# Kernel tuning notes

Measured on AMD Instinct MI355X. Metric: run time of the kernel, lower is better.

Reference implementation:

```python
import jax, jax.numpy as jnp
import numpy as np

B, N, D, DV, FS, SE, TPH = 4096, 50, 128, 8, 4, 20, 64
NEG = -1e9
C_CLIP = 10.0  # pointer Attention use_tanh with C=10


def setup_inputs():
    key = jax.random.key(0)
    ks = jax.random.split(key, 24)
    r = lambda i, shape, s=1.0: jax.random.normal(ks[i], shape, jnp.float32) * s
    return dict(
        decoder_input=r(0, (B, D)),
        h0=r(1, (B, D)),
        c0=r(2, (B, D)),
        V_reach_mask=jnp.zeros((B, N), bool),
        start_idx=jax.random.randint(ks[3], (B,), 0, N),
        V=r(4, (B, N, DV)),
        b_E=r(5, (B, N, N)),
        b_E_abs=r(6, (B, N, N)),
        context_update=r(7, (N, B, D)),
        H_update=r(8, (B, N, D - 2)),
        start_fea=r(9, (B, FS)),
        # LSTMCell params (torch gate order i,f,g,o)
        W_ih=r(10, (4 * D, D), 0.05), W_hh=r(11, (4 * D, D), 0.05),
        b_ih=jnp.zeros(4 * D), b_hh=jnp.zeros(4 * D),
        # glimpse Attention
        gWq=r(12, (D, D), 0.05), gbq=jnp.zeros(D),
        gWr=r(13, (D, D), 0.05), gbr=jnp.zeros(D), gv=r(14, (D,), 0.05),
        # pointer Attention
        pWq=r(15, (D, D), 0.05), pbq=jnp.zeros(D),
        pWr=r(16, (D, D), 0.05), pbr=jnp.zeros(D), pv=r(17, (D,), 0.05),
        # step embedding table [max_task_num+1, 20]
        step_table=r(18, (N + 1, SE), 0.05),
        # net_TP MLP: Linear(40,64)+ReLU+Linear(64,1)
        tp_W1=r(19, (2 * DV + FS + SE, TPH), 0.05), tp_b1=jnp.zeros(TPH),
        tp_W2=r(20, (TPH, 1), 0.05), tp_b2=jnp.zeros(1),
    )


def _mask_modify(m):
    # if a row is all True, un-mask the last column
    return m.at[:, -1].set(jnp.where(m.all(axis=1), False, m[:, -1]))


def _decode(decoder_input, h0, c0, V, context_update, start_fea,
            W_ih, W_hh, b_ih, b_hh,
            gWq, gbq, gWr, gbr, gv, pWq, pbq, pWr, pbr, pv,
            step_table, tp_W1, tp_b1, tp_W2, tp_b2,
            V_reach_mask, start_idx):
    ar_b = jnp.arange(B)
    # project_ref (1x1 conv) on the fixed context: precompute once
    e_g = jnp.einsum('de,nbe->bnd', gWr, context_update) + gbr  # [B,N,D]
    e_p = jnp.einsum('de,nbe->bnd', pWr, context_update) + pbr  # [B,N,D]

    def step(carry, t):
        h, c, mask, prev, last, x = carry
        scat = mask.at[ar_b, prev].set(True)
        m = jnp.where(t == 0, _mask_modify(mask), _mask_modify(scat))
        # LSTMCell
        gates = x @ W_ih.T + b_ih + h @ W_hh.T + b_hh
        i_, f_, g_, o_ = jnp.split(gates, 4, axis=-1)
        c2 = jax.nn.sigmoid(f_) * c + jax.nn.sigmoid(i_) * jnp.tanh(g_)
        h2 = jax.nn.sigmoid(o_) * jnp.tanh(c2)
        # glimpse (n_glimpses=1, masked)
        qg = h2 @ gWq.T + gbq
        ug = jnp.einsum('d,bnd->bn', gv, jnp.tanh(qg[:, None, :] + e_g))
        ug = jnp.where(m, NEG, ug)
        gl = jnp.einsum('bnd,bn->bd', e_g, jax.nn.softmax(ug, axis=1))
        # pointer (tanh-clipped, masked)
        qp = gl @ pWq.T + pbq
        up = jnp.einsum('d,bnd->bn', pv, jnp.tanh(qp[:, None, :] + e_p))
        logits = jnp.where(m, NEG, C_CLIP * jnp.tanh(up))
        log_p = jax.nn.log_softmax(logits, axis=1)
        idxs = jnp.argmax(log_p, axis=1)
        # time-prediction features + MLP
        se = jnp.broadcast_to(step_table[t], (B, SE))
        tp_in = jnp.concatenate([V[ar_b, last], V[ar_b, idxs], start_fea, se], axis=1)
        pred = jax.nn.relu(tp_in @ tp_W1 + tp_b1) @ tp_W2 + tp_b2  # [B,1]
        # rp_update_features: next decoder input gathered from fixed context
        x2 = context_update[idxs, ar_b]
        return (h2, c2, m, idxs, idxs, x2), (log_p, idxs, pred[:, 0])

    init = (h0, c0, V_reach_mask, jnp.zeros(B, jnp.int32),
            start_idx.astype(jnp.int32), decoder_input)
    _, (lp, sel, pt) = jax.lax.scan(step, init, jnp.arange(N))
    return jnp.transpose(lp, (1, 0, 2)), sel.T, pt.T  # [B,T,N],[B,T],[B,T]


def reference(decoder_input, h0, c0, V_reach_mask, start_idx, V, b_E, b_E_abs,
              context_update, H_update, start_fea,
              W_ih, W_hh, b_ih, b_hh,
              gWq, gbq, gWr, gbr, gv, pWq, pbq, pWr, pbr, pv,
              step_table, tp_W1, tp_b1, tp_W2, tp_b2):
    log_probs, selections, pred_t = _decode(
        decoder_input, h0, c0, V, context_update, start_fea,
        W_ih, W_hh, b_ih, b_hh,
        gWq, gbq, gWr, gbr, gv, pWq, pbq, pWr, pbr, pv,
        step_table, tp_W1, tp_b1, tp_W2, tp_b2,
        V_reach_mask, start_idx)
    # (output_prob, selections, time_duration_pred, pred_eta)
    return log_probs, selections, pred_t, pred_t[..., None]
```

## Files before the change

### kernel.cpp

```cpp
#include <hip/hip_runtime.h>
#include <math.h>

#define B_   4096
#define N_   50
#define D_   128
#define DV_  8
#define FS_  4
#define SE_  20
#define TPH_ 64
#define NEGV (-1e9f)
#define G_   16
#define NBLK (B_ / G_)

__device__ __forceinline__ float frcp_(float x) { return __builtin_amdgcn_rcpf(x); }
__device__ __forceinline__ float ftanh_(float x) {
    float e = __expf(2.f * x);
    return 1.f - 2.f * frcp_(e + 1.f);
}
__device__ __forceinline__ float fsig_(float x) {
    return frcp_(1.f + __expf(-x));
}
__device__ __forceinline__ float wsum_(float v) {
#pragma unroll
    for (int m = 1; m < 64; m <<= 1) v += __shfl_xor(v, m);
    return v;
}

__global__ __launch_bounds__(256) void proj_kernel(
    const float* __restrict__ W,
    const float* __restrict__ bias,
    const float* __restrict__ cu,
    float* __restrict__ outp)
{
    __shared__ __align__(16) float scu[20][128];
    __shared__ float sb[128];
    const int tid = threadIdx.x;
    if (tid < 128) sb[tid] = bias[tid];
    const int d  = tid & 127;
    const int rq = tid >> 7;
    const float* wrow = W + d * 128;
    const int r0 = blockIdx.x * 200;
    for (int it = 0; it < 10; ++it) {
        const int rbase = r0 + it * 20;
        __syncthreads();
        for (int i = tid; i < 20 * 128; i += 256) {
            int rr = i >> 7, e = i & 127;
            int r = rbase + rr;
            int b = r / 50, n = r - b * 50;
            scu[rr][e] = cu[((size_t)n * B_ + b) * D_ + e];
        }
        __syncthreads();
        float acc[10];
#pragma unroll
        for (int k = 0; k < 10; ++k) acc[k] = 0.f;
        const int rr0 = rq * 10;
        for (int e = 0; e < 128; e += 4) {
            float4 w4 = *(const float4*)&wrow[e];
#pragma unroll
            for (int k = 0; k < 10; ++k) {
                float4 c4 = *(const float4*)&scu[rr0 + k][e];
                acc[k] += w4.x * c4.x + w4.y * c4.y + w4.z * c4.z + w4.w * c4.w;
            }
        }
        float bv = sb[d];
#pragma unroll
        for (int k = 0; k < 10; ++k)
            outp[(size_t)(rbase + rr0 + k) * D_ + d] = acc[k] + bv;
    }
}

__global__ __launch_bounds__(256) void transpose_kernel(
    const float* __restrict__ in, float* __restrict__ out, int R, int C)
{
    int idx = blockIdx.x * 256 + threadIdx.x;
    if (idx < R * C) {
        int r = idx / C, c = idx - r * C;
        out[c * R + r] = in[idx];
    }
}

#define PF_ 10

__global__ __launch_bounds__(1024, 4) void decode_kernel(
    const float* __restrict__ dec_in,
    const float* __restrict__ h0,
    const float* __restrict__ c0,
    const unsigned char* __restrict__ vmask,
    const int* __restrict__ start_idx,
    const float* __restrict__ V,
    const float* __restrict__ cu,
    const float* __restrict__ start_fea,
    const float* __restrict__ W_ih,
    const float* __restrict__ W_hh,
    const float* __restrict__ b_ih, const float* __restrict__ b_hh,
    const float* __restrict__ gWq, const float* __restrict__ gbq,
    const float* __restrict__ gv,
    const float* __restrict__ pWq, const float* __restrict__ pbq,
    const float* __restrict__ pv,
    const float* __restrict__ step_table,
    const float* __restrict__ tpW1, const float* __restrict__ tpb1,
    const float* __restrict__ tpW2, const float* __restrict__ tpb2,
    const float* __restrict__ e_g, const float* __restrict__ e_p,
    const float* __restrict__ wtI,
    const float* __restrict__ wtH,
    const float* __restrict__ gqT,
    const float* __restrict__ pqT,
    const int use_t,
    float* __restrict__ outp)
{
    __shared__ __align__(16) float sH[G_][D_];
    __shared__ __align__(16) float sC[G_][D_];
    __shared__ __align__(16) float sX[G_][D_];
    __shared__ __align__(16) float sU[G_ * 512];
    __shared__ __align__(16) float sP2[G_ * 512];
    __shared__ float sBias[512];
    __shared__ __align__(16) float sGbq[128];
    __shared__ __align__(16) float sPbq[128];
    __shared__ __align__(16) float sGv[128];
    __shared__ __align__(16) float sPv[128];
    __shared__ float sSF[G_][FS_];
    __shared__ unsigned long long sMaskC[G_];
    __shared__ int sPrev[G_], sLast[G_];

    const int tid = threadIdx.x;
    const int b0  = blockIdx.x * G_;

    for (int i = tid; i < G_ * D_; i += 1024) {
        int g = i >> 7, d = i & 127;
        size_t src = (size_t)(b0 + g) * D_ + d;
        sH[g][d] = h0[src];
        sC[g][d] = c0[src];
        sX[g][d] = dec_in[src];
    }
    if (tid < 512)       sBias[tid]      = b_ih[tid] + b_hh[tid];
    else if (tid < 640)  sGbq[tid - 512] = gbq[tid - 512];
    else if (tid < 768)  sPbq[tid - 640] = pbq[tid - 640];
    else if (tid < 896)  sGv[tid - 768]  = gv[tid - 768];
    else                 sPv[tid - 896]  = pv[tid - 896];
    if (tid < G_ * FS_) {
        int g = tid >> 2, k = tid & 3;
        sSF[g][k] = start_fea[(size_t)(b0 + g) * FS_ + k];
    }
    if (tid < G_) {
        unsigned long long mk = 0ull;
        const unsigned char* mrow = vmask + (size_t)(b0 + tid) * N_;
        for (int n = 0; n < N_; ++n)
            if (mrow[n]) mk |= (1ull << n);
        sMaskC[tid] = mk;
        sPrev[tid]  = 0;
        sLast[tid]  = start_idx[b0 + tid];
    }
    __syncthreads();

    const unsigned long long FULL = (1ull << N_) - 1ull;

    for (int t = 0; t < N_; ++t) {
        if (tid < G_) {
            unsigned long long mk = sMaskC[tid];
            if (t > 0) mk |= (1ull << sPrev[tid]);
            if ((mk & FULL) == FULL) mk &= ~(1ull << (N_ - 1));
            sMaskC[tid] = mk;
        }
        if (use_t) {
            const int j  = tid & 511;
            const int eh = tid >> 9;
            const int ebase = eh * 64;
            const float* wI = wtI + j;
            const float* wH = wtH + j;
            float acc[16];
#pragma unroll
            for (int g = 0; g < 16; ++g) acc[g] = 0.f;
#pragma unroll 2
            for (int ec = 0; ec < 64; ec += 4) {
                const int e = ebase + ec;
                float wi0 = wI[(size_t)(e + 0) * 512], wi1 = wI[(size_t)(e + 1) * 512];
                float wi2 = wI[(size_t)(e + 2) * 512], wi3 = wI[(size_t)(e + 3) * 512];
                float wh0 = wH[(size_t)(e + 0) * 512], wh1 = wH[(size_t)(e + 1) * 512];
                float wh2 = wH[(size_t)(e + 2) * 512], wh3 = wH[(size_t)(e + 3) * 512];
#pragma unroll
                for (int g = 0; g < 16; ++g) {
                    float4 x4 = *(const float4*)&sX[g][e];
                    float4 h4 = *(const float4*)&sH[g][e];
                    acc[g] += wi0 * x4.x + wi1 * x4.y + wi2 * x4.z + wi3 * x4.w
                            + wh0 * h4.x + wh1 * h4.y + wh2 * h4.z + wh3 * h4.w;
                }
            }
            if (eh == 0) {
                float bb = sBias[j];
#pragma unroll
                for (int g = 0; g < 16; ++g) sU[g * 512 + j] = acc[g] + bb;
            } else {
#pragma unroll
                for (int g = 0; g < 16; ++g) sP2[g * 512 + j] = acc[g];
            }
        } else {
            const int j  = tid & 511;
            const int gh = tid >> 9;
            const int gbase = gh * 8;
            const float* wih = W_ih + (size_t)j * 128;
            const float* whh = W_hh + (size_t)j * 128;
            float acc[8];
#pragma unroll
            for (int g = 0; g < 8; ++g) acc[g] = 0.f;
            for (int e = 0; e < 128; e += 16) {
                float4 wi[4], wh[4];
#pragma unroll
                for (int q = 0; q < 4; ++q) {
                    wi[q] = *(const float4*)&wih[e + 4 * q];
                    wh[q] = *(const float4*)&whh[e + 4 * q];
                }
#pragma unroll
                for (int g = 0; g < 8; ++g) {
                    const float* xr = &sX[gbase + g][e];
                    const float* hr = &sH[gbase + g][e];
#pragma unroll
                    for (int q = 0; q < 4; ++q) {
                        float4 x4 = *(const float4*)&xr[4 * q];
                        float4 h4 = *(const float4*)&hr[4 * q];
                        acc[g] += wi[q].x * x4.x + wi[q].y * x4.y + wi[q].z * x4.z + wi[q].w * x4.w
                                + wh[q].x * h4.x + wh[q].y * h4.y + wh[q].z * h4.z + wh[q].w * h4.w;
                    }
                }
            }
            float bb = sBias[j];
#pragma unroll
            for (int g = 0; g < 8; ++g) sU[(gbase + g) * 512 + j] = acc[g] + bb;
        }
        __syncthreads();

        for (int i = tid; i < G_ * D_; i += 1024) {
            int g = i >> 7, d = i & 127;
            float u0 = sU[g * 512 + d],       u1 = sU[g * 512 + 128 + d];
            float u2 = sU[g * 512 + 256 + d], u3 = sU[g * 512 + 384 + d];
            if (use_t) {
                u0 += sP2[g * 512 + d];       u1 += sP2[g * 512 + 128 + d];
                u2 += sP2[g * 512 + 256 + d]; u3 += sP2[g * 512 + 384 + d];
            }
            float ig = fsig_(u0);
            float fg = fsig_(u1);
            float gg = ftanh_(u2);
            float og = fsig_(u3);
            float c2 = fg * sC[g][d] + ig * gg;
            sC[g][d] = c2;
            sH[g][d] = og * ftanh_(c2);
        }
        __syncthreads();

        if (use_t) {
            const int d  = tid & 127;
            const int gh = tid >> 7;
            const int g0 = gh * 2;
            const float* wq = gqT + d;
            float a0 = 0.f, a1 = 0.f;
#pragma unroll 4
            for (int e = 0; e < 128; e += 4) {
                float w0 = wq[(e + 0) * 128], w1 = wq[(e + 1) * 128];
                float w2 = wq[(e + 2) * 128], w3 = wq[(e + 3) * 128];
                float4 hA = *(const float4*)&sH[g0][e];
                float4 hB = *(const float4*)&sH[g0 + 1][e];
                a0 += w0 * hA.x + w1 * hA.y + w2 * hA.z + w3 * hA.w;
                a1 += w0 * hB.x + w1 * hB.y + w2 * hB.z + w3 * hB.w;
            }
            sU[g0 * 128 + d]       = a0 + sGbq[d];
            sU[(g0 + 1) * 128 + d] = a1 + sGbq[d];
        } else {
            const int d  = tid & 127;
            const int gh = tid >> 7;
            const int g0 = gh * 2;
            const float* wr = gWq + (size_t)d * 128;
            float a0 = 0.f, a1 = 0.f;
            for (int e = 0; e < 128; e += 16) {
                float4 w4[4];
#pragma unroll
                for (int q = 0; q < 4; ++q) w4[q] = *(const float4*)&wr[e + 4 * q];
#pragma unroll
                for (int q = 0; q < 4; ++q) {
                    float4 hA = *(const float4*)&sH[g0][e + 4 * q];
                    float4 hB = *(const float4*)&sH[g0 + 1][e + 4 * q];
                    a0 += w4[q].x * hA.x + w4[q].y * hA.y + w4[q].z * hA.z + w4[q].w * hA.w;
                    a1 += w4[q].x * hB.x + w4[q].y * hB.y + w4[q].z * hB.z + w4[q].w * hB.w;
                }
            }
            sU[g0 * 128 + d]       = a0 + sGbq[d];
            sU[(g0 + 1) * 128 + d] = a1 + sGbq[d];
        }
        __syncthreads();

        {
            const int g = tid >> 6;
            const int lane = tid & 63;
            const int b = b0 + g;
            const float qg1 = sU[g * 128 + lane];
            const float qg2 = sU[g * 128 + 64 + lane];
            const float gv1 = sGv[lane], gv2 = sGv[64 + lane];
            const unsigned long long mk = sMaskC[g];
            const float* egb = e_g + (size_t)b * (N_ * D_);
            float l = 0.f, a1 = 0.f, a2 = 0.f;
            float r1[PF_], r2[PF_];
#pragma unroll
            for (int p = 0; p < PF_; ++p) {
                r1[p] = egb[p * 128 + lane];
                r2[p] = egb[p * 128 + 64 + lane];
            }
#pragma unroll
            for (int n = 0; n < N_; ++n) {
                const int s = n % PF_;
                float c1 = r1[s], c2 = r2[s];
                if (n + PF_ < N_) {
                    r1[s] = egb[(n + PF_) * 128 + lane];
                    r2[s] = egb[(n + PF_) * 128 + 64 + lane];
                }
                float part = gv1 * ftanh_(qg1 + c1) + gv2 * ftanh_(qg2 + c2);
                float u = wsum_(part);
                float w = ((mk >> n) & 1ull) ? 0.f : __expf(u);
                l  += w;
                a1 += w * c1;
                a2 += w * c2;
            }
            float inv = 1.f / l;
            sU[2048 + g * 128 + lane]      = a1 * inv;
            sU[2048 + g * 128 + 64 + lane] = a2 * inv;
        }
        __syncthreads();

        if (use_t) {
            const int d  = tid & 127;
            const int gh = tid >> 7;
            const int g0 = gh * 2;
            const float* wq = pqT + d;
            float a0 = 0.f, a1 = 0.f;
#pragma unroll 4
            for (int e = 0; e < 128; e += 4) {
                float w0 = wq[(e + 0) * 128], w1 = wq[(e + 1) * 128];
                float w2 = wq[(e + 2) * 128], w3 = wq[(e + 3) * 128];
                float4 hA = *(const float4*)&sU[2048 + g0 * 128 + e];
                float4 hB = *(const float4*)&sU[2048 + (g0 + 1) * 128 + e];
                a0 += w0 * hA.x + w1 * hA.y + w2 * hA.z + w3 * hA.w;
                a1 += w0 * hB.x + w1 * hB.y + w2 * hB.z + w3 * hB.w;
            }
            sU[g0 * 128 + d]       = a0 + sPbq[d];
            sU[(g0 + 1) * 128 + d] = a1 + sPbq[d];
        } else {
            const int d  = tid & 127;
            const int gh = tid >> 7;
            const int g0 = gh * 2;
            const float* wr = pWq + (size_t)d * 128;
            float a0 = 0.f, a1 = 0.f;
            for (int e = 0; e < 128; e += 16) {
                float4 w4[4];
#pragma unroll
                for (int q = 0; q < 4; ++q) w4[q] = *(const float4*)&wr[e + 4 * q];
#pragma unroll
                for (int q = 0; q < 4; ++q) {
                    float4 hA = *(const float4*)&sU[2048 + g0 * 128 + e + 4 * q];
                    float4 hB = *(const float4*)&sU[2048 + (g0 + 1) * 128 + e + 4 * q];
                    a0 += w4[q].x * hA.x + w4[q].y * hA.y + w4[q].z * hA.z + w4[q].w * hA.w;
                    a1 += w4[q].x * hB.x + w4[q].y * hB.y + w4[q].z * hB.z + w4[q].w * hB.w;
                }
            }
            sU[g0 * 128 + d]       = a0 + sPbq[d];
            sU[(g0 + 1) * 128 + d] = a1 + sPbq[d];
        }
        __syncthreads();

        {
            const int g = tid >> 6;
            const int lane = tid & 63;
            const int b = b0 + g;
            const unsigned long long mk = sMaskC[g];
            const float qpa = sU[g * 128 + lane];
            const float qpb = sU[g * 128 + 64 + lane];
            const float pva = sPv[lane], pvb = sPv[64 + lane];
            const float* epb = e_p + (size_t)b * (N_ * D_);
            float logit = -__builtin_inff();
            float r1[PF_], r2[PF_];
#pragma unroll
            for (int p = 0; p < PF_; ++p) {
                r1[p] = epb[p * 128 + lane];
                r2[p] = epb[p * 128 + 64 + lane];
            }
#pragma unroll
            for (int n = 0; n < N_; ++n) {
                const int s = n % PF_;
                float c1 = r1[s], c2 = r2[s];
                if (n + PF_ < N_) {
                    r1[s] = epb[(n + PF_) * 128 + lane];
                    r2[s] = epb[(n + PF_) * 128 + 64 + lane];
                }
                float part = pva * ftanh_(qpa + c1) + pvb * ftanh_(qpb + c2);
                float u = wsum_(part);
                float tl = ((mk >> n) & 1ull) ? NEGV : 10.0f * ftanh_(u);
                logit = (lane == n) ? tl : logit;
            }
            const bool active = lane < N_;
            float mx = logit;
#pragma unroll
            for (int mm = 1; mm < 64; mm <<= 1) mx = fmaxf(mx, __shfl_xor(mx, mm));
            float ex = active ? __expf(logit - mx) : 0.f;
            float s = wsum_(ex);
            float lse = mx + __logf(s);
            if (active)
                __builtin_nontemporal_store(logit - lse,
                    &outp[(size_t)b * (N_ * N_) + t * N_ + lane]);
            float av = logit; int ai = active ? lane : (N_ - 1);
#pragma unroll
            for (int mm = 1; mm < 64; mm <<= 1) {
                float ov = __shfl_xor(av, mm);
                int   oi = __shfl_xor(ai, mm);
                bool take = (ov > av) || (ov == av && oi < ai);
                av = take ? ov : av;
                ai = take ? oi : ai;
            }
            const int idx = ai;
            const int lastv = sLast[g];
            const float* Vl = V + ((size_t)b * N_ + lastv) * DV_;
            const float* Vi = V + ((size_t)b * N_ + idx) * DV_;
            float hacc = tpb1[lane];
#pragma unroll
            for (int k = 0; k < 8; ++k)  hacc += Vl[k] * tpW1[k * 64 + lane];
#pragma unroll
            for (int k = 0; k < 8; ++k)  hacc += Vi[k] * tpW1[(8 + k) * 64 + lane];
#pragma unroll
            for (int k = 0; k < 4; ++k)  hacc += sSF[g][k] * tpW1[(16 + k) * 64 + lane];
#pragma unroll
            for (int k = 0; k < 20; ++k) hacc += step_table[t * SE_ + k] * tpW1[(20 + k) * 64 + lane];
            hacc = fmaxf(hacc, 0.f);
            float pred = wsum_(hacc * tpW2[lane]) + tpb2[0];
            const float* xrow = cu + ((size_t)idx * B_ + b) * D_;
            sX[g][lane]      = xrow[lane];
            sX[g][64 + lane] = xrow[64 + lane];
            if (lane == 0) {
                __builtin_nontemporal_store((float)idx,
                    &outp[(size_t)(B_ * N_) * N_ + (size_t)b * N_ + t]);
                __builtin_nontemporal_store(pred,
                    &outp[(size_t)(B_ * N_) * N_ + (size_t)(B_ * N_) + (size_t)b * N_ + t]);
                __builtin_nontemporal_store(pred,
                    &outp[(size_t)(B_ * N_) * N_ + 2 * (size_t)(B_ * N_) + (size_t)b * N_ + t]);
                sPrev[g] = idx;
                sLast[g] = idx;
            }
        }
        __syncthreads();
    }
}

extern "C" void kernel_launch(void* const* d_in, const int* in_sizes, int n_in,
                              void* d_out, int out_size, void* d_ws, size_t ws_size,
                              hipStream_t stream)
{
    const float* dec   = (const float*)d_in[0];
    const float* h0    = (const float*)d_in[1];
    const float* c0    = (const float*)d_in[2];
    const unsigned char* vmask = (const unsigned char*)d_in[3];
    const int*   sidx  = (const int*)d_in[4];
    const float* V     = (const float*)d_in[5];
    const float* cu    = (const float*)d_in[8];
    const float* sfea  = (const float*)d_in[10];
    const float* W_ih  = (const float*)d_in[11];
    const float* W_hh  = (const float*)d_in[12];
    const float* b_ih  = (const float*)d_in[13];
    const float* b_hh  = (const float*)d_in[14];
    const float* gWq   = (const float*)d_in[15];
    const float* gbq   = (const float*)d_in[16];
    const float* gWr   = (const float*)d_in[17];
    const float* gbr   = (const float*)d_in[18];
    const float* gv    = (const float*)d_in[19];
    const float* pWq   = (const float*)d_in[20];
    const float* pbq   = (const float*)d_in[21];
    const float* pWr   = (const float*)d_in[22];
    const float* pbr   = (const float*)d_in[23];
    const float* pv    = (const float*)d_in[24];
    const float* stept = (const float*)d_in[25];
    const float* tpW1  = (const float*)d_in[26];
    const float* tpb1  = (const float*)d_in[27];
    const float* tpW2  = (const float*)d_in[28];
    const float* tpb2  = (const float*)d_in[29];

    const size_t EG = (size_t)B_ * N_ * D_;
    float* e_g = (float*)d_ws;
    float* e_p = e_g + EG;

    float* wtI = e_p + EG;
    float* wtH = wtI + 512 * 128;
    float* gqT = wtH + 512 * 128;
    float* pqT = gqT + 128 * 128;
    const size_t need = (2 * EG + 2 * (512 * 128) + 2 * (128 * 128)) * sizeof(float);
    const int use_t = (ws_size >= need) ? 1 : 0;

    proj_kernel<<<dim3(1024), 256, 0, stream>>>(gWr, gbr, cu, e_g);
    proj_kernel<<<dim3(1024), 256, 0, stream>>>(pWr, pbr, cu, e_p);
    if (use_t) {
        transpose_kernel<<<dim3(256), 256, 0, stream>>>(W_ih, wtI, 512, 128);
        transpose_kernel<<<dim3(256), 256, 0, stream>>>(W_hh, wtH, 512, 128);
        transpose_kernel<<<dim3(64),  256, 0, stream>>>(gWq,  gqT, 128, 128);
        transpose_kernel<<<dim3(64),  256, 0, stream>>>(pWq,  pqT, 128, 128);
    }
    decode_kernel<<<dim3(NBLK), 1024, 0, stream>>>(
        dec, h0, c0, vmask, sidx, V, cu, sfea,
        W_ih, W_hh, b_ih, b_hh,
        gWq, gbq, gv, pWq, pbq, pv,
        stept, tpW1, tpb1, tpW2, tpb2,
        e_g, e_p, wtI, wtH, gqT, pqT, use_t, (float*)d_out);
}
```

Measured before the change: 7.378 ms.

## Repartition attention loops: 4 nodes per wave with 8-wide d slices

```diff
diff --git a/kernel.cpp b/kernel.cpp
--- a/kernel.cpp
+++ b/kernel.cpp
@@ -79,7 +79,7 @@
     }
 }
 
-#define PF_ 10
+#define NB4_ 13
 
 __global__ __launch_bounds__(1024, 4) void decode_kernel(
     const float* __restrict__ dec_in,
@@ -119,6 +119,7 @@
     __shared__ __align__(16) float sGv[128];
     __shared__ __align__(16) float sPv[128];
     __shared__ float sSF[G_][FS_];
+    __shared__ float sLg[G_][64];
     __shared__ unsigned long long sMaskC[G_];
     __shared__ int sPrev[G_], sLast[G_];
 
@@ -246,6 +247,17 @@
         }
         __syncthreads();
 
+        const int gW   = tid >> 6;
+        const int lane = tid & 63;
+        const int nq   = lane >> 4;
+        const int dh   = lane & 15;
+        const float* egb = e_g + (size_t)(b0 + gW) * (N_ * D_) + dh * 8;
+        const float* epb = e_p + (size_t)(b0 + gW) * (N_ * D_) + dh * 8;
+
+        float4 pgA0 = *(const float4*)&egb[(size_t)nq * 128];
+        float4 pgB0 = *(const float4*)&egb[(size_t)nq * 128 + 4];
+        float4 pgA1 = *(const float4*)&egb[(size_t)(4 + nq) * 128];
+        float4 pgB1 = *(const float4*)&egb[(size_t)(4 + nq) * 128 + 4];
         if (use_t) {
             const int d  = tid & 127;
             const int gh = tid >> 7;
@@ -287,42 +299,61 @@
         __syncthreads();
 
         {
-            const int g = tid >> 6;
-            const int lane = tid & 63;
-            const int b = b0 + g;
-            const float qg1 = sU[g * 128 + lane];
-            const float qg2 = sU[g * 128 + 64 + lane];
-            const float gv1 = sGv[lane], gv2 = sGv[64 + lane];
-            const unsigned long long mk = sMaskC[g];
-            const float* egb = e_g + (size_t)b * (N_ * D_);
-            float l = 0.f, a1 = 0.f, a2 = 0.f;
-            float r1[PF_], r2[PF_];
-#pragma unroll
-            for (int p = 0; p < PF_; ++p) {
-                r1[p] = egb[p * 128 + lane];
-                r2[p] = egb[p * 128 + 64 + lane];
-            }
-#pragma unroll
-            for (int n = 0; n < N_; ++n) {
-                const int s = n % PF_;
-                float c1 = r1[s], c2 = r2[s];
-                if (n + PF_ < N_) {
-                    r1[s] = egb[(n + PF_) * 128 + lane];
-                    r2[s] = egb[(n + PF_) * 128 + 64 + lane];
-                }
-                float part = gv1 * ftanh_(qg1 + c1) + gv2 * ftanh_(qg2 + c2);
-                float u = wsum_(part);
-                float w = ((mk >> n) & 1ull) ? 0.f : __expf(u);
-                l  += w;
-                a1 += w * c1;
-                a2 += w * c2;
+            const unsigned long long mk = sMaskC[gW];
+            float qgv[8], gvv[8];
+            *(float4*)&qgv[0] = *(const float4*)&sU[gW * 128 + dh * 8];
+            *(float4*)&qgv[4] = *(const float4*)&sU[gW * 128 + dh * 8 + 4];
+            *(float4*)&gvv[0] = *(const float4*)&sGv[dh * 8];
+            *(float4*)&gvv[4] = *(const float4*)&sGv[dh * 8 + 4];
+            float l = 0.f;
+            float a[8];
+#pragma unroll
+            for (int j = 0; j < 8; ++j) a[j] = 0.f;
+#pragma unroll
+            for (int blk = 0; blk < NB4_; ++blk) {
+                const int n = blk * 4 + nq;
+                const int nn = (n < N_) ? n : (N_ - 1);
+                float4 cA, cB;
+                if (blk == 0)      { cA = pgA0; cB = pgB0; }
+                else if (blk == 1) { cA = pgA1; cB = pgB1; }
+                else {
+                    cA = *(const float4*)&egb[(size_t)nn * 128];
+                    cB = *(const float4*)&egb[(size_t)nn * 128 + 4];
+                }
+                float c[8] = {cA.x, cA.y, cA.z, cA.w, cB.x, cB.y, cB.z, cB.w};
+                float part = 0.f;
+#pragma unroll
+                for (int j = 0; j < 8; ++j) part += gvv[j] * ftanh_(qgv[j] + c[j]);
+                part += __shfl_xor(part, 1);
+                part += __shfl_xor(part, 2);
+                part += __shfl_xor(part, 4);
+                part += __shfl_xor(part, 8);
+                const bool dead = (n >= N_) || ((mk >> n) & 1ull);
+                float w = dead ? 0.f : __expf(part);
+                l += w;
+#pragma unroll
+                for (int j = 0; j < 8; ++j) a[j] += w * c[j];
+            }
+#pragma unroll
+            for (int mmk = 16; mmk < 64; mmk <<= 1) {
+                l += __shfl_xor(l, mmk);
+#pragma unroll
+                for (int j = 0; j < 8; ++j) a[j] += __shfl_xor(a[j], mmk);
             }
             float inv = 1.f / l;
-            sU[2048 + g * 128 + lane]      = a1 * inv;
-            sU[2048 + g * 128 + 64 + lane] = a2 * inv;
-        }
-        __syncthreads();
-
+            if (nq == 0) {
+                float4 o1 = {a[0] * inv, a[1] * inv, a[2] * inv, a[3] * inv};
+                float4 o2 = {a[4] * inv, a[5] * inv, a[6] * inv, a[7] * inv};
+                *(float4*)&sU[2048 + gW * 128 + dh * 8]     = o1;
+                *(float4*)&sU[2048 + gW * 128 + dh * 8 + 4] = o2;
+            }
+        }
+        __syncthreads();
+
+        float4 ppA0 = *(const float4*)&epb[(size_t)nq * 128];
+        float4 ppB0 = *(const float4*)&epb[(size_t)nq * 128 + 4];
+        float4 ppA1 = *(const float4*)&epb[(size_t)(4 + nq) * 128];
+        float4 ppB1 = *(const float4*)&epb[(size_t)(4 + nq) * 128 + 4];
         if (use_t) {
             const int d  = tid & 127;
             const int gh = tid >> 7;
@@ -364,35 +395,42 @@
         __syncthreads();
 
         {
-            const int g = tid >> 6;
-            const int lane = tid & 63;
-            const int b = b0 + g;
-            const unsigned long long mk = sMaskC[g];
-            const float qpa = sU[g * 128 + lane];
-            const float qpb = sU[g * 128 + 64 + lane];
-            const float pva = sPv[lane], pvb = sPv[64 + lane];
-            const float* epb = e_p + (size_t)b * (N_ * D_);
-            float logit = -__builtin_inff();
-            float r1[PF_], r2[PF_];
-#pragma unroll
-            for (int p = 0; p < PF_; ++p) {
-                r1[p] = epb[p * 128 + lane];
-                r2[p] = epb[p * 128 + 64 + lane];
-            }
-#pragma unroll
-            for (int n = 0; n < N_; ++n) {
-                const int s = n % PF_;
-                float c1 = r1[s], c2 = r2[s];
-                if (n + PF_ < N_) {
-                    r1[s] = epb[(n + PF_) * 128 + lane];
-                    r2[s] = epb[(n + PF_) * 128 + 64 + lane];
-                }
-                float part = pva * ftanh_(qpa + c1) + pvb * ftanh_(qpb + c2);
-                float u = wsum_(part);
-                float tl = ((mk >> n) & 1ull) ? NEGV : 10.0f * ftanh_(u);
-                logit = (lane == n) ? tl : logit;
+            const int b = b0 + gW;
+            const unsigned long long mk = sMaskC[gW];
+            {
+                float qpv[8], pvv[8];
+                *(float4*)&qpv[0] = *(const float4*)&sU[gW * 128 + dh * 8];
+                *(float4*)&qpv[4] = *(const float4*)&sU[gW * 128 + dh * 8 + 4];
+                *(float4*)&pvv[0] = *(const float4*)&sPv[dh * 8];
+                *(float4*)&pvv[4] = *(const float4*)&sPv[dh * 8 + 4];
+#pragma unroll
+                for (int blk = 0; blk < NB4_; ++blk) {
+                    const int n = blk * 4 + nq;
+                    const int nn = (n < N_) ? n : (N_ - 1);
+                    float4 cA, cB;
+                    if (blk == 0)      { cA = ppA0; cB = ppB0; }
+                    else if (blk == 1) { cA = ppA1; cB = ppB1; }
+                    else {
+                        cA = *(const float4*)&epb[(size_t)nn * 128];
+                        cB = *(const float4*)&epb[(size_t)nn * 128 + 4];
+                    }
+                    float c[8] = {cA.x, cA.y, cA.z, cA.w, cB.x, cB.y, cB.z, cB.w};
+                    float part = 0.f;
+#pragma unroll
+                    for (int j = 0; j < 8; ++j) part += pvv[j] * ftanh_(qpv[j] + c[j]);
+                    part += __shfl_xor(part, 1);
+                    part += __shfl_xor(part, 2);
+                    part += __shfl_xor(part, 4);
+                    part += __shfl_xor(part, 8);
+                    if (dh == 0 && n < N_) {
+                        float tl = ((mk >> n) & 1ull) ? NEGV : 10.0f * ftanh_(part);
+                        sLg[gW][n] = tl;
+                    }
+                }
             }
             const bool active = lane < N_;
+            float lgv = sLg[gW][lane];
+            float logit = active ? lgv : -__builtin_inff();
             float mx = logit;
 #pragma unroll
             for (int mm = 1; mm < 64; mm <<= 1) mx = fmaxf(mx, __shfl_xor(mx, mm));
@@ -412,7 +450,7 @@
                 ai = take ? oi : ai;
             }
             const int idx = ai;
-            const int lastv = sLast[g];
+            const int lastv = sLast[gW];
             const float* Vl = V + ((size_t)b * N_ + lastv) * DV_;
             const float* Vi = V + ((size_t)b * N_ + idx) * DV_;
             float hacc = tpb1[lane];
@@ -421,14 +459,14 @@
 #pragma unroll
             for (int k = 0; k < 8; ++k)  hacc += Vi[k] * tpW1[(8 + k) * 64 + lane];
 #pragma unroll
-            for (int k = 0; k < 4; ++k)  hacc += sSF[g][k] * tpW1[(16 + k) * 64 + lane];
+            for (int k = 0; k < 4; ++k)  hacc += sSF[gW][k] * tpW1[(16 + k) * 64 + lane];
 #pragma unroll
             for (int k = 0; k < 20; ++k) hacc += step_table[t * SE_ + k] * tpW1[(20 + k) * 64 + lane];
             hacc = fmaxf(hacc, 0.f);
             float pred = wsum_(hacc * tpW2[lane]) + tpb2[0];
             const float* xrow = cu + ((size_t)idx * B_ + b) * D_;
-            sX[g][lane]      = xrow[lane];
-            sX[g][64 + lane] = xrow[64 + lane];
+            sX[gW][lane]      = xrow[lane];
+            sX[gW][64 + lane] = xrow[64 + lane];
             if (lane == 0) {
                 __builtin_nontemporal_store((float)idx,
                     &outp[(size_t)(B_ * N_) * N_ + (size_t)b * N_ + t]);
@@ -436,8 +474,8 @@
                     &outp[(size_t)(B_ * N_) * N_ + (size_t)(B_ * N_) + (size_t)b * N_ + t]);
                 __builtin_nontemporal_store(pred,
                     &outp[(size_t)(B_ * N_) * N_ + 2 * (size_t)(B_ * N_) + (size_t)b * N_ + t]);
-                sPrev[g] = idx;
-                sLast[g] = idx;
+                sPrev[gW] = idx;
+                sLast[gW] = idx;
             }
         }
         __syncthreads();
```

Measured after the change: 7.158 ms. 1.03x faster.

## Make each wavefront own one batch row to drop block barriers per step

Applied to the files above, without the earlier changes.

```diff
diff --git a/kernel.cpp b/kernel.cpp
--- a/kernel.cpp
+++ b/kernel.cpp
@@ -78,8 +78,6 @@
         out[c * R + r] = in[idx];
     }
 }
-
-#define PF_ 10
 
 __global__ __launch_bounds__(1024, 4) void decode_kernel(
     const float* __restrict__ dec_in,
@@ -113,24 +111,28 @@
     __shared__ __align__(16) float sX[G_][D_];
     __shared__ __align__(16) float sU[G_ * 512];
     __shared__ __align__(16) float sP2[G_ * 512];
+    __shared__ __align__(16) float sQ[G_][D_];
+    __shared__ __align__(16) float sGl[G_][D_];
+    __shared__ float sLg[G_][64];
     __shared__ float sBias[512];
     __shared__ __align__(16) float sGbq[128];
     __shared__ __align__(16) float sPbq[128];
     __shared__ __align__(16) float sGv[128];
     __shared__ __align__(16) float sPv[128];
     __shared__ float sSF[G_][FS_];
-    __shared__ unsigned long long sMaskC[G_];
-    __shared__ int sPrev[G_], sLast[G_];
-
-    const int tid = threadIdx.x;
-    const int b0  = blockIdx.x * G_;
+
+    const int tid  = threadIdx.x;
+    const int b0   = blockIdx.x * G_;
+    const int g    = tid >> 6;
+    const int lane = tid & 63;
+    const int b    = b0 + g;
 
     for (int i = tid; i < G_ * D_; i += 1024) {
-        int g = i >> 7, d = i & 127;
-        size_t src = (size_t)(b0 + g) * D_ + d;
-        sH[g][d] = h0[src];
-        sC[g][d] = c0[src];
-        sX[g][d] = dec_in[src];
+        int gg = i >> 7, d = i & 127;
+        size_t src = (size_t)(b0 + gg) * D_ + d;
+        sH[gg][d] = h0[src];
+        sC[gg][d] = c0[src];
+        sX[gg][d] = dec_in[src];
     }
     if (tid < 512)       sBias[tid]      = b_ih[tid] + b_hh[tid];
     else if (tid < 640)  sGbq[tid - 512] = gbq[tid - 512];
@@ -138,29 +140,20 @@
     else if (tid < 896)  sGv[tid - 768]  = gv[tid - 768];
     else                 sPv[tid - 896]  = pv[tid - 896];
     if (tid < G_ * FS_) {
-        int g = tid >> 2, k = tid & 3;
-        sSF[g][k] = start_fea[(size_t)(b0 + g) * FS_ + k];
-    }
-    if (tid < G_) {
-        unsigned long long mk = 0ull;
-        const unsigned char* mrow = vmask + (size_t)(b0 + tid) * N_;
-        for (int n = 0; n < N_; ++n)
-            if (mrow[n]) mk |= (1ull << n);
-        sMaskC[tid] = mk;
-        sPrev[tid]  = 0;
-        sLast[tid]  = start_idx[b0 + tid];
-    }
+        int gg = tid >> 2, k = tid & 3;
+        sSF[gg][k] = start_fea[(size_t)(b0 + gg) * FS_ + k];
+    }
+    unsigned char mv = (lane < N_) ? vmask[(size_t)b * N_ + lane] : (unsigned char)0;
+    unsigned long long mk = __ballot(mv != 0);
+    int lastv = start_idx[b];
+    int prev  = 0;
     __syncthreads();
 
     const unsigned long long FULL = (1ull << N_) - 1ull;
+    const int nh = lane >> 5;
+    const int dq = lane & 31;
 
     for (int t = 0; t < N_; ++t) {
-        if (tid < G_) {
-            unsigned long long mk = sMaskC[tid];
-            if (t > 0) mk |= (1ull << sPrev[tid]);
-            if ((mk & FULL) == FULL) mk &= ~(1ull << (N_ - 1));
-            sMaskC[tid] = mk;
-        }
         if (use_t) {
             const int j  = tid & 511;
             const int eh = tid >> 9;
@@ -169,7 +162,7 @@
             const float* wH = wtH + j;
             float acc[16];
 #pragma unroll
-            for (int g = 0; g < 16; ++g) acc[g] = 0.f;
+            for (int q = 0; q < 16; ++q) acc[q] = 0.f;
 #pragma unroll 2
             for (int ec = 0; ec < 64; ec += 4) {
                 const int e = ebase + ec;
@@ -178,20 +171,20 @@
                 float wh0 = wH[(size_t)(e + 0) * 512], wh1 = wH[(size_t)(e + 1) * 512];
                 float wh2 = wH[(size_t)(e + 2) * 512], wh3 = wH[(size_t)(e + 3) * 512];
 #pragma unroll
-                for (int g = 0; g < 16; ++g) {
-                    float4 x4 = *(const float4*)&sX[g][e];
-                    float4 h4 = *(const float4*)&sH[g][e];
-                    acc[g] += wi0 * x4.x + wi1 * x4.y + wi2 * x4.z + wi3 * x4.w
+                for (int q = 0; q < 16; ++q) {
+                    float4 x4 = *(const float4*)&sX[q][e];
+                    float4 h4 = *(const float4*)&sH[q][e];
+                    acc[q] += wi0 * x4.x + wi1 * x4.y + wi2 * x4.z + wi3 * x4.w
                             + wh0 * h4.x + wh1 * h4.y + wh2 * h4.z + wh3 * h4.w;
                 }
             }
             if (eh == 0) {
                 float bb = sBias[j];
 #pragma unroll
-                for (int g = 0; g < 16; ++g) sU[g * 512 + j] = acc[g] + bb;
+                for (int q = 0; q < 16; ++q) sU[q * 512 + j] = acc[q] + bb;
             } else {
 #pragma unroll
-                for (int g = 0; g < 16; ++g) sP2[g * 512 + j] = acc[g];
+                for (int q = 0; q < 16; ++q) sP2[q * 512 + j] = acc[q];
             }
         } else {
             const int j  = tid & 511;
@@ -201,198 +194,176 @@
             const float* whh = W_hh + (size_t)j * 128;
             float acc[8];
 #pragma unroll
-            for (int g = 0; g < 8; ++g) acc[g] = 0.f;
+            for (int q = 0; q < 8; ++q) acc[q] = 0.f;
             for (int e = 0; e < 128; e += 16) {
                 float4 wi[4], wh[4];
 #pragma unroll
-                for (int q = 0; q < 4; ++q) {
-                    wi[q] = *(const float4*)&wih[e + 4 * q];
-                    wh[q] = *(const float4*)&whh[e + 4 * q];
+                for (int w = 0; w < 4; ++w) {
+                    wi[w] = *(const float4*)&wih[e + 4 * w];
+                    wh[w] = *(const float4*)&whh[e + 4 * w];
                 }
 #pragma unroll
-                for (int g = 0; g < 8; ++g) {
-                    const float* xr = &sX[gbase + g][e];
-                    const float* hr = &sH[gbase + g][e];
-#pragma unroll
-                    for (int q = 0; q < 4; ++q) {
-                        float4 x4 = *(const float4*)&xr[4 * q];
-                        float4 h4 = *(const float4*)&hr[4 * q];
-                        acc[g] += wi[q].x * x4.x + wi[q].y * x4.y + wi[q].z * x4.z + wi[q].w * x4.w
-                                + wh[q].x * h4.x + wh[q].y * h4.y + wh[q].z * h4.z + wh[q].w * h4.w;
+                for (int q = 0; q < 8; ++q) {
+                    const float* xr = &sX[gbase + q][e];
+                    const float* hr = &sH[gbase + q][e];
+#pragma unroll
+                    for (int w = 0; w < 4; ++w) {
+                        float4 x4 = *(const float4*)&xr[4 * w];
+                        float4 h4 = *(const float4*)&hr[4 * w];
+                        acc[q] += wi[w].x * x4.x + wi[w].y * x4.y + wi[w].z * x4.z + wi[w].w * x4.w
+                                + wh[w].x * h4.x + wh[w].y * h4.y + wh[w].z * h4.z + wh[w].w * h4.w;
                     }
                 }
             }
             float bb = sBias[j];
 #pragma unroll
-            for (int g = 0; g < 8; ++g) sU[(gbase + g) * 512 + j] = acc[g] + bb;
+            for (int q = 0; q < 8; ++q) sU[(gbase + q) * 512 + j] = acc[q] + bb;
         }
         __syncthreads();
 
-        for (int i = tid; i < G_ * D_; i += 1024) {
-            int g = i >> 7, d = i & 127;
+#pragma unroll
+        for (int h = 0; h < 2; ++h) {
+            const int d = lane + h * 64;
             float u0 = sU[g * 512 + d],       u1 = sU[g * 512 + 128 + d];
             float u2 = sU[g * 512 + 256 + d], u3 = sU[g * 512 + 384 + d];
             if (use_t) {
                 u0 += sP2[g * 512 + d];       u1 += sP2[g * 512 + 128 + d];
                 u2 += sP2[g * 512 + 256 + d]; u3 += sP2[g * 512 + 384 + d];
             }
-            float ig = fsig_(u0);
-            float fg = fsig_(u1);
-            float gg = ftanh_(u2);
-            float og = fsig_(u3);
-            float c2 = fg * sC[g][d] + ig * gg;
+            float ig = fsig_(u0), fg = fsig_(u1), gg2 = ftanh_(u2), og = fsig_(u3);
+            float c2 = fg * sC[g][d] + ig * gg2;
             sC[g][d] = c2;
             sH[g][d] = og * ftanh_(c2);
         }
-        __syncthreads();
+        if (t > 0) mk |= (1ull << prev);
+        if ((mk & FULL) == FULL) mk &= ~(1ull << (N_ - 1));
 
         if (use_t) {
-            const int d  = tid & 127;
-            const int gh = tid >> 7;
-            const int g0 = gh * 2;
-            const float* wq = gqT + d;
+            const float* wq = gqT + 2 * lane;
             float a0 = 0.f, a1 = 0.f;
-#pragma unroll 4
+#pragma unroll 8
             for (int e = 0; e < 128; e += 4) {
-                float w0 = wq[(e + 0) * 128], w1 = wq[(e + 1) * 128];
-                float w2 = wq[(e + 2) * 128], w3 = wq[(e + 3) * 128];
-                float4 hA = *(const float4*)&sH[g0][e];
-                float4 hB = *(const float4*)&sH[g0 + 1][e];
-                a0 += w0 * hA.x + w1 * hA.y + w2 * hA.z + w3 * hA.w;
-                a1 += w0 * hB.x + w1 * hB.y + w2 * hB.z + w3 * hB.w;
-            }
-            sU[g0 * 128 + d]       = a0 + sGbq[d];
-            sU[(g0 + 1) * 128 + d] = a1 + sGbq[d];
+                float4 h4 = *(const float4*)&sH[g][e];
+                float2 w0 = *(const float2*)&wq[(size_t)(e + 0) * 128];
+                float2 w1 = *(const float2*)&wq[(size_t)(e + 1) * 128];
+                float2 w2 = *(const float2*)&wq[(size_t)(e + 2) * 128];
+                float2 w3 = *(const float2*)&wq[(size_t)(e + 3) * 128];
+                a0 += w0.x * h4.x + w1.x * h4.y + w2.x * h4.z + w3.x * h4.w;
+                a1 += w0.y * h4.x + w1.y * h4.y + w2.y * h4.z + w3.y * h4.w;
+            }
+            sQ[g][2 * lane]     = a0 + sGbq[2 * lane];
+            sQ[g][2 * lane + 1] = a1 + sGbq[2 * lane + 1];
         } else {
-            const int d  = tid & 127;
-            const int gh = tid >> 7;
-            const int g0 = gh * 2;
-            const float* wr = gWq + (size_t)d * 128;
+            const float* w0r = gWq + (size_t)(2 * lane) * 128;
+            const float* w1r = w0r + 128;
             float a0 = 0.f, a1 = 0.f;
-            for (int e = 0; e < 128; e += 16) {
-                float4 w4[4];
-#pragma unroll
-                for (int q = 0; q < 4; ++q) w4[q] = *(const float4*)&wr[e + 4 * q];
-#pragma unroll
-                for (int q = 0; q < 4; ++q) {
-                    float4 hA = *(const float4*)&sH[g0][e + 4 * q];
-                    float4 hB = *(const float4*)&sH[g0 + 1][e + 4 * q];
-                    a0 += w4[q].x * hA.x + w4[q].y * hA.y + w4[q].z * hA.z + w4[q].w * hA.w;
-                    a1 += w4[q].x * hB.x + w4[q].y * hB.y + w4[q].z * hB.z + w4[q].w * hB.w;
+            for (int e = 0; e < 128; e += 4) {
+                float4 h4 = *(const float4*)&sH[g][e];
+                float4 wa = *(const float4*)&w0r[e];
+                float4 wb = *(const float4*)&w1r[e];
+                a0 += wa.x * h4.x + wa.y * h4.y + wa.z * h4.z + wa.w * h4.w;
+                a1 += wb.x * h4.x + wb.y * h4.y + wb.z * h4.z + wb.w * h4.w;
+            }
+            sQ[g][2 * lane]     = a0 + sGbq[2 * lane];
+            sQ[g][2 * lane + 1] = a1 + sGbq[2 * lane + 1];
+        }
+
+        {
+            float4 qg4 = *(const float4*)&sQ[g][dq * 4];
+            float4 gv4 = *(const float4*)&sGv[dq * 4];
+            const float* egb = e_g + (size_t)b * (N_ * D_) + nh * D_ + dq * 4;
+            float4 p0 = *(const float4*)&egb[0 * 256];
+            float4 p1 = *(const float4*)&egb[1 * 256];
+            float4 p2 = *(const float4*)&egb[2 * 256];
+            float4 p3 = *(const float4*)&egb[3 * 256];
+            float l = 0.f;
+            float4 acc = {0.f, 0.f, 0.f, 0.f};
+#pragma unroll
+            for (int blk = 0; blk < 25; ++blk) {
+                float4 c = p0; p0 = p1; p1 = p2; p2 = p3;
+                if (blk + 4 < 25) p3 = *(const float4*)&egb[(size_t)(blk + 4) * 256];
+                float part = gv4.x * ftanh_(qg4.x + c.x) + gv4.y * ftanh_(qg4.y + c.y)
+                           + gv4.z * ftanh_(qg4.z + c.z) + gv4.w * ftanh_(qg4.w + c.w);
+                part += __shfl_xor(part, 1);
+                part += __shfl_xor(part, 2);
+                part += __shfl_xor(part, 4);
+                part += __shfl_xor(part, 8);
+                part += __shfl_xor(part, 16);
+                const int n = 2 * blk + nh;
+                float w = ((mk >> n) & 1ull) ? 0.f : __expf(part);
+                l += w;
+                acc.x += w * c.x; acc.y += w * c.y; acc.z += w * c.z; acc.w += w * c.w;
+            }
+            l     += __shfl_xor(l, 32);
+            acc.x += __shfl_xor(acc.x, 32);
+            acc.y += __shfl_xor(acc.y, 32);
+            acc.z += __shfl_xor(acc.z, 32);
+            acc.w += __shfl_xor(acc.w, 32);
+            float inv = 1.f / l;
+            if (nh == 0) {
+                float4 o = {acc.x * inv, acc.y * inv, acc.z * inv, acc.w * inv};
+                *(float4*)&sGl[g][dq * 4] = o;
+            }
+        }
+
+        if (use_t) {
+            const float* wq = pqT + 2 * lane;
+            float a0 = 0.f, a1 = 0.f;
+#pragma unroll 8
+            for (int e = 0; e < 128; e += 4) {
+                float4 h4 = *(const float4*)&sGl[g][e];
+                float2 w0 = *(const float2*)&wq[(size_t)(e + 0) * 128];
+                float2 w1 = *(const float2*)&wq[(size_t)(e + 1) * 128];
+                float2 w2 = *(const float2*)&wq[(size_t)(e + 2) * 128];
+                float2 w3 = *(const float2*)&wq[(size_t)(e + 3) * 128];
+                a0 += w0.x * h4.x + w1.x * h4.y + w2.x * h4.z + w3.x * h4.w;
+                a1 += w0.y * h4.x + w1.y * h4.y + w2.y * h4.z + w3.y * h4.w;
+            }
+            sQ[g][2 * lane]     = a0 + sPbq[2 * lane];
+            sQ[g][2 * lane + 1] = a1 + sPbq[2 * lane + 1];
+        } else {
+            const float* w0r = pWq + (size_t)(2 * lane) * 128;
+            const float* w1r = w0r + 128;
+            float a0 = 0.f, a1 = 0.f;
+            for (int e = 0; e < 128; e += 4) {
+                float4 h4 = *(const float4*)&sGl[g][e];
+                float4 wa = *(const float4*)&w0r[e];
+                float4 wb = *(const float4*)&w1r[e];
+                a0 += wa.x * h4.x + wa.y * h4.y + wa.z * h4.z + wa.w * h4.w;
+                a1 += wb.x * h4.x + wb.y * h4.y + wb.z * h4.z + wb.w * h4.w;
+            }
+            sQ[g][2 * lane]     = a0 + sPbq[2 * lane];
+            sQ[g][2 * lane + 1] = a1 + sPbq[2 * lane + 1];
+        }
+
+        {
+            float4 qp4 = *(const float4*)&sQ[g][dq * 4];
+            float4 pv4 = *(const float4*)&sPv[dq * 4];
+            const float* epb = e_p + (size_t)b * (N_ * D_) + nh * D_ + dq * 4;
+            float4 p0 = *(const float4*)&epb[0 * 256];
+            float4 p1 = *(const float4*)&epb[1 * 256];
+            float4 p2 = *(const float4*)&epb[2 * 256];
+            float4 p3 = *(const float4*)&epb[3 * 256];
+#pragma unroll
+            for (int blk = 0; blk < 25; ++blk) {
+                float4 c = p0; p0 = p1; p1 = p2; p2 = p3;
+                if (blk + 4 < 25) p3 = *(const float4*)&epb[(size_t)(blk + 4) * 256];
+                float part = pv4.x * ftanh_(qp4.x + c.x) + pv4.y * ftanh_(qp4.y + c.y)
+                           + pv4.z * ftanh_(qp4.z + c.z) + pv4.w * ftanh_(qp4.w + c.w);
+                part += __shfl_xor(part, 1);
+                part += __shfl_xor(part, 2);
+                part += __shfl_xor(part, 4);
+                part += __shfl_xor(part, 8);
+                part += __shfl_xor(part, 16);
+                const int n = 2 * blk + nh;
+                if (dq == 0) {
+                    float tl = ((mk >> n) & 1ull) ? NEGV : 10.0f * ftanh_(part);
+                    sLg[g][n] = tl;
                 }
             }
-            sU[g0 * 128 + d]       = a0 + sGbq[d];
-            sU[(g0 + 1) * 128 + d] = a1 + sGbq[d];
-        }
-        __syncthreads();
-
-        {
-            const int g = tid >> 6;
-            const int lane = tid & 63;
-            const int b = b0 + g;
-            const float qg1 = sU[g * 128 + lane];
-            const float qg2 = sU[g * 128 + 64 + lane];
-            const float gv1 = sGv[lane], gv2 = sGv[64 + lane];
-            const unsigned long long mk = sMaskC[g];
-            const float* egb = e_g + (size_t)b * (N_ * D_);
-            float l = 0.f, a1 = 0.f, a2 = 0.f;
-            float r1[PF_], r2[PF_];
-#pragma unroll
-            for (int p = 0; p < PF_; ++p) {
-                r1[p] = egb[p * 128 + lane];
-                r2[p] = egb[p * 128 + 64 + lane];
-            }
-#pragma unroll
-            for (int n = 0; n < N_; ++n) {
-                const int s = n % PF_;
-                float c1 = r1[s], c2 = r2[s];
-                if (n + PF_ < N_) {
-                    r1[s] = egb[(n + PF_) * 128 + lane];
-                    r2[s] = egb[(n + PF_) * 128 + 64 + lane];
-                }
-                float part = gv1 * ftanh_(qg1 + c1) + gv2 * ftanh_(qg2 + c2);
-                float u = wsum_(part);
-                float w = ((mk >> n) & 1ull) ? 0.f : __expf(u);
-                l  += w;
-                a1 += w * c1;
-                a2 += w * c2;
-            }
-            float inv = 1.f / l;
-            sU[2048 + g * 128 + lane]      = a1 * inv;
-            sU[2048 + g * 128 + 64 + lane] = a2 * inv;
-        }
-        __syncthreads();
-
-        if (use_t) {
-            const int d  = tid & 127;
-            const int gh = tid >> 7;
-            const int g0 = gh * 2;
-            const float* wq = pqT + d;
-            float a0 = 0.f, a1 = 0.f;
-#pragma unroll 4
-            for (int e = 0; e < 128; e += 4) {
-                float w0 = wq[(e + 0) * 128], w1 = wq[(e + 1) * 128];
-                float w2 = wq[(e + 2) * 128], w3 = wq[(e + 3) * 128];
-                float4 hA = *(const float4*)&sU[2048 + g0 * 128 + e];
-                float4 hB = *(const float4*)&sU[2048 + (g0 + 1) * 128 + e];
-                a0 += w0 * hA.x + w1 * hA.y + w2 * hA.z + w3 * hA.w;
-                a1 += w0 * hB.x + w1 * hB.y + w2 * hB.z + w3 * hB.w;
-            }
-            sU[g0 * 128 + d]       = a0 + sPbq[d];
-            sU[(g0 + 1) * 128 + d] = a1 + sPbq[d];
-        } else {
-            const int d  = tid & 127;
-            const int gh = tid >> 7;
-            const int g0 = gh * 2;
-            const float* wr = pWq + (size_t)d * 128;
-            float a0 = 0.f, a1 = 0.f;
-            for (int e = 0; e < 128; e += 16) {
-                float4 w4[4];
-#pragma unroll
-                for (int q = 0; q < 4; ++q) w4[q] = *(const float4*)&wr[e + 4 * q];
-#pragma unroll
-                for (int q = 0; q < 4; ++q) {
-                    float4 hA = *(const float4*)&sU[2048 + g0 * 128 + e + 4 * q];
-                    float4 hB = *(const float4*)&sU[2048 + (g0 + 1) * 128 + e + 4 * q];
-                    a0 += w4[q].x * hA.x + w4[q].y * hA.y + w4[q].z * hA.z + w4[q].w * hA.w;
-                    a1 += w4[q].x * hB.x + w4[q].y * hB.y + w4[q].z * hB.z + w4[q].w * hB.w;
-                }
-            }
-            sU[g0 * 128 + d]       = a0 + sPbq[d];
-            sU[(g0 + 1) * 128 + d] = a1 + sPbq[d];
-        }
-        __syncthreads();
-
-        {
-            const int g = tid >> 6;
-            const int lane = tid & 63;
-            const int b = b0 + g;
-            const unsigned long long mk = sMaskC[g];
-            const float qpa = sU[g * 128 + lane];
-            const float qpb = sU[g * 128 + 64 + lane];
-            const float pva = sPv[lane], pvb = sPv[64 + lane];
-            const float* epb = e_p + (size_t)b * (N_ * D_);
-            float logit = -__builtin_inff();
-            float r1[PF_], r2[PF_];
-#pragma unroll
-            for (int p = 0; p < PF_; ++p) {
-                r1[p] = epb[p * 128 + lane];
-                r2[p] = epb[p * 128 + 64 + lane];
-            }
-#pragma unroll
-            for (int n = 0; n < N_; ++n) {
-                const int s = n % PF_;
-                float c1 = r1[s], c2 = r2[s];
-                if (n + PF_ < N_) {
-                    r1[s] = epb[(n + PF_) * 128 + lane];
-                    r2[s] = epb[(n + PF_) * 128 + 64 + lane];
-                }
-                float part = pva * ftanh_(qpa + c1) + pvb * ftanh_(qpb + c2);
-                float u = wsum_(part);
-                float tl = ((mk >> n) & 1ull) ? NEGV : 10.0f * ftanh_(u);
-                logit = (lane == n) ? tl : logit;
-            }
             const bool active = lane < N_;
+            float lgv = sLg[g][lane];
+            float logit = active ? lgv : -__builtin_inff();
             float mx = logit;
 #pragma unroll
             for (int mm = 1; mm < 64; mm <<= 1) mx = fmaxf(mx, __shfl_xor(mx, mm));
@@ -412,7 +383,6 @@
                 ai = take ? oi : ai;
             }
             const int idx = ai;
-            const int lastv = sLast[g];
             const float* Vl = V + ((size_t)b * N_ + lastv) * DV_;
             const float* Vi = V + ((size_t)b * N_ + idx) * DV_;
             float hacc = tpb1[lane];
@@ -436,9 +406,9 @@
                     &outp[(size_t)(B_ * N_) * N_ + (size_t)(B_ * N_) + (size_t)b * N_ + t]);
                 __builtin_nontemporal_store(pred,
                     &outp[(size_t)(B_ * N_) * N_ + 2 * (size_t)(B_ * N_) + (size_t)b * N_ + t]);
-                sPrev[g] = idx;
-                sLast[g] = idx;
-            }
+            }
+            prev  = idx;
+            lastv = idx;
         }
         __syncthreads();
     }
```

Result: slower. 8.431 ms (+14.3%).
